# Kernel tuning notes

Measured on AMD Instinct MI355X. Metric: run time of the kernel, lower is better.

Reference implementation:

```python
import jax, jax.numpy as jnp
import numpy as np


def setup_inputs() -> dict:
    key = jax.random.key(0)
    ks = jax.random.split(key, 5)
    B, S, D = 2, 2048, 1024
    inv = 1.0 / np.sqrt(D)
    inp = {
        "x": jax.random.normal(ks[0], (B, S, D), jnp.float32),
        "Wq": jax.random.normal(ks[1], (D, D), jnp.float32) * inv,
        "bq": jnp.zeros((D,), jnp.float32),
        "Wk": jax.random.normal(ks[2], (D, D), jnp.float32) * inv,
        "bk": jnp.zeros((D,), jnp.float32),
        "Wv": jax.random.normal(ks[3], (D, D), jnp.float32) * inv,
        "bv": jnp.zeros((D,), jnp.float32),
        "Wo": jax.random.normal(ks[4], (D, D), jnp.float32) * inv,
        "bo": jnp.zeros((D,), jnp.float32),
        "num_heads": 16,
        "window_size": 128,
    }
    return inp


def reference(x, Wq, bq, Wk, bk, Wv, bv, Wo, bo, num_heads, window_size):
    B, S, D = x.shape
    H = num_heads
    hd = D // H
    scale = 1.0 / np.sqrt(hd)

    def split_heads(t):  # [B,S,D] -> [B,H,S,hd]
        return t.reshape(B, S, H, hd).transpose(0, 2, 1, 3)

    q = split_heads(x @ Wq + bq)
    k = split_heads(x @ Wk + bk)
    v = split_heads(x @ Wv + bv)

    # dense scores, then sliding-window + causal mask (faithful to original)
    scores = jnp.einsum('bhqd,bhkd->bhqk', q, k) * scale  # [B,H,S,S]
    i = jnp.arange(S)[:, None]
    j = jnp.arange(S)[None, :]
    # position i attends to j in [i - window_size + 1, i]
    mask = (j <= i) & (j > i - window_size)
    scores = jnp.where(mask, scores, -jnp.inf)
    attn_weights = jax.nn.softmax(scores, axis=-1)  # dropout is identity in eval

    out = jnp.einsum('bhqk,bhkd->bhqd', attn_weights, v)  # [B,H,S,hd]
    out = out.transpose(0, 2, 1, 3).reshape(B, S, D)
    return out @ Wo + bo, attn_weights
```

## Files before the change

### kernel.cpp

```cpp
#include <hip/hip_runtime.h>
#include <cmath>

typedef __attribute__((ext_vector_type(8))) __bf16 v8bf;
typedef __attribute__((ext_vector_type(4))) float  v4f;

#define DEV static __device__ __forceinline__

DEV unsigned short f2bf(float f) {
  unsigned u = __builtin_bit_cast(unsigned, f);
  unsigned r = u + 0x7fffu + ((u >> 16) & 1u);
  return (unsigned short)(r >> 16);
}
DEV float bf2f(unsigned short s) {
  return __builtin_bit_cast(float, ((unsigned)s) << 16);
}
DEV v8bf ld8(const unsigned short* p) { return *(const v8bf*)p; }

DEV void gl16(const unsigned short* g, unsigned short* l) {
  __builtin_amdgcn_global_load_lds(
      (const __attribute__((address_space(1))) unsigned int*)g,
      (__attribute__((address_space(3))) unsigned int*)l, 16, 0, 0);
}

__global__ __launch_bounds__(256) void k_prep(const float* __restrict__ x,
                                              const float* __restrict__ Wq,
                                              const float* __restrict__ Wk,
                                              const float* __restrict__ Wv,
                                              const float* __restrict__ Wo,
                                              const float* __restrict__ bq,
                                              const float* __restrict__ bk,
                                              const float* __restrict__ bv,
                                              unsigned short* __restrict__ xb,
                                              unsigned short* __restrict__ WT,
                                              unsigned short* __restrict__ WoT,
                                              float* __restrict__ bqkv) {
  __shared__ float t[32][33];
  int bx = blockIdx.x, tid = threadIdx.x;
  if (bx < 4096) {
    int i = bx * 256 + tid;
    float4 v = ((const float4*)x)[i];
    unsigned lo = (unsigned)f2bf(v.x) | ((unsigned)f2bf(v.y) << 16);
    unsigned hi = (unsigned)f2bf(v.z) | ((unsigned)f2bf(v.w) << 16);
    ((uint2*)xb)[i] = make_uint2(lo, hi);
  } else if (bx < 8192) {
    int rem = bx - 4096;
    int z = rem >> 10, r2 = rem & 1023;
    const float* src = (z == 0) ? Wq : (z == 1) ? Wk : (z == 2) ? Wv : Wo;
    unsigned short* dst = (z < 3) ? WT + z * 1048576 : WoT;
    int n0 = (r2 & 31) * 32, k0 = (r2 >> 5) * 32;
    int tx = tid & 31, ty = tid >> 5;
    for (int r = ty; r < 32; r += 8)
      t[r][tx] = src[(k0 + r) * 1024 + n0 + tx];
    __syncthreads();
    for (int r = ty; r < 32; r += 8)
      dst[(n0 + r) * 1024 + k0 + tx] = f2bf(t[tx][r]);
  } else {
    int i = (bx - 8192) * 256 + tid;
    float v = (i < 1024) ? bq[i] : (i < 2048 ? bk[i - 1024] : bv[i - 2048]);
    bqkv[i] = v;
  }
}

__global__ __launch_bounds__(256) void k_gemm1(const unsigned short* __restrict__ A,
                                               const unsigned short* __restrict__ Bt,
                                               const float* __restrict__ bias,
                                               unsigned short* __restrict__ Cout) {
  constexpr int K = 1024;
  __shared__ __attribute__((aligned(16))) unsigned short As[128 * 32];
  __shared__ __attribute__((aligned(16))) unsigned short Bs[128 * 32];
  int tid = threadIdx.x;
  int wave = tid >> 6, lane = tid & 63;
  int m0 = blockIdx.y * 128, n0 = blockIdx.x * 128;
  int wm = (wave >> 1) * 64, wn = (wave & 1) * 64;
  int m = lane & 15, q4 = lane >> 4;
  int arow = tid >> 2, acol = (tid & 3) * 8;
  v4f acc[4][4] = {};
  const unsigned short* ga0 = A + (m0 + arow) * K + acol;
  const unsigned short* ga1 = A + (m0 + 64 + arow) * K + acol;
  const unsigned short* gb0 = Bt + (n0 + arow) * K + acol;
  const unsigned short* gb1 = Bt + (n0 + 64 + arow) * K + acol;
  unsigned short* lA0 = As + wave * 512;
  unsigned short* lA1 = As + 2048 + wave * 512;
  unsigned short* lB0 = Bs + wave * 512;
  unsigned short* lB1 = Bs + 2048 + wave * 512;

  for (int kt = 0; kt < K; kt += 32) {
    gl16(ga0 + kt, lA0);
    gl16(ga1 + kt, lA1);
    gl16(gb0 + kt, lB0);
    gl16(gb1 + kt, lB1);
    __syncthreads();
    v8bf af[4], bfv[4];
#pragma unroll
    for (int mt = 0; mt < 4; mt++) af[mt] = ld8(&As[(wm + mt * 16 + m) * 32 + q4 * 8]);
#pragma unroll
    for (int nt = 0; nt < 4; nt++) bfv[nt] = ld8(&Bs[(wn + nt * 16 + m) * 32 + q4 * 8]);
#pragma unroll
    for (int mt = 0; mt < 4; mt++)
#pragma unroll
      for (int nt = 0; nt < 4; nt++)
        acc[mt][nt] = __builtin_amdgcn_mfma_f32_16x16x32_bf16(af[mt], bfv[nt], acc[mt][nt], 0, 0, 0);
    __syncthreads();
  }
#pragma unroll
  for (int mt = 0; mt < 4; mt++)
#pragma unroll
    for (int nt = 0; nt < 4; nt++) {
      int col = n0 + wn + nt * 16 + m;
      float bb = bias[col];
#pragma unroll
      for (int r = 0; r < 4; r++) {
        int row = m0 + wm + mt * 16 + q4 * 4 + r;
        Cout[row * 3072 + col] = f2bf(acc[mt][nt][r] + bb);
      }
    }
}

__global__ __launch_bounds__(256) void k_transv(const unsigned short* __restrict__ QKV,
                                                unsigned short* __restrict__ Vtg) {
  __shared__ unsigned short t[32][33];
  int bx = blockIdx.x, tid = threadIdx.x;
  int st = bx & 63, h2 = (bx >> 6) & 1, bh = bx >> 7;
  int b = bh >> 4, h = bh & 15;
  int s0 = st * 32, d0 = h2 * 32;
  int tx = tid & 31, ty = tid >> 5;
  const unsigned short* src = QKV + (size_t)b * 2048 * 3072 + 2048 + h * 64 + d0;
  for (int r = ty; r < 32; r += 8)
    t[r][tx] = src[(size_t)(s0 + r) * 3072 + tx];
  __syncthreads();
  unsigned short* dst = Vtg + (size_t)(bh * 64 + d0) * 2048 + s0;
  for (int r = ty; r < 32; r += 8)
    dst[(size_t)r * 2048 + tx] = t[tx][r];
}

__global__ __launch_bounds__(256) void k_attn(const unsigned short* __restrict__ QKV,
                                              const unsigned short* __restrict__ Vtg,
                                              unsigned short* __restrict__ Oatt,
                                              unsigned short* __restrict__ cb) {
  constexpr int VTS = 208;
  constexpr int PSS = 168;
  __shared__ __attribute__((aligned(16))) unsigned short Vt[64 * VTS];
  __shared__ __attribute__((aligned(16))) unsigned short Ps[4][16 * PSS];
  int b = blockIdx.z, h = blockIdx.y, i0 = blockIdx.x * 64;
  int tid = threadIdx.x, wave = tid >> 6, lane = tid & 63;
  int kbase = i0 - 128;
  const int ld = 3072;
  const unsigned short* Qg = QKV + b * 2048 * ld + h * 64;
  const unsigned short* Kg = Qg + 1024;

  const unsigned short* vsrc = Vtg + (size_t)(b * 16 + h) * 64 * 2048;
  for (int idx = tid; idx < 1536; idx += 256) {
    int row = idx / 24, c16 = idx % 24;
    int gcol = kbase + c16 * 8;
    if (gcol < 0) gcol = 0;
    v8bf vv = ld8(vsrc + (size_t)row * 2048 + gcol);
    *(v8bf*)&Vt[row * VTS + c16 * 8] = vv;
  }
  {
    int row = tid >> 2, c4 = (tid & 3) * 4;
    *(uint2*)&Vt[row * VTS + 192 + c4] = make_uint2(0u, 0u);
  }
  for (int c = lane; c < 16 * 24; c += 64)
    Ps[wave][(c / 24) * PSS + 144 + (c % 24)] = 0;
  __syncthreads();

  int qb = i0 + wave * 16;
  int m = lane & 15, q4 = lane >> 4;

  const unsigned short* qrow = Qg + (qb + m) * ld;
  v8bf qa0 = ld8(qrow + q4 * 8);
  v8bf qa1 = ld8(qrow + 32 + q4 * 8);

  v4f sc[9];
#pragma unroll
  for (int n = 0; n < 9; n++) {
    int key = kbase + wave * 16 + n * 16 + m;
    int kg = key < 0 ? 0 : key;
    const unsigned short* krow = Kg + kg * ld;
    v8bf kb0 = ld8(krow + q4 * 8);
    v8bf kb1 = ld8(krow + 32 + q4 * 8);
    v4f z = {0.f, 0.f, 0.f, 0.f};
    z = __builtin_amdgcn_mfma_f32_16x16x32_bf16(qa0, kb0, z, 0, 0, 0);
    z = __builtin_amdgcn_mfma_f32_16x16x32_bf16(qa1, kb1, z, 0, 0, 0);
    sc[n] = z;
  }
  float mx[4] = {-3e38f, -3e38f, -3e38f, -3e38f};
#pragma unroll
  for (int n = 0; n < 9; n++)
#pragma unroll
    for (int r = 0; r < 4; r++) {
      int i = qb + q4 * 4 + r;
      int j = kbase + wave * 16 + n * 16 + m;
      float v = sc[n][r] * 0.125f;
      bool ok = (j >= 0) && (j <= i) && (j > i - 128);
      v = ok ? v : -3e38f;
      sc[n][r] = v;
      mx[r] = fmaxf(mx[r], v);
    }
#pragma unroll
  for (int o = 1; o < 16; o <<= 1)
#pragma unroll
    for (int r = 0; r < 4; r++) mx[r] = fmaxf(mx[r], __shfl_xor(mx[r], o, 64));
  float sum[4] = {0.f, 0.f, 0.f, 0.f};
#pragma unroll
  for (int n = 0; n < 9; n++)
#pragma unroll
    for (int r = 0; r < 4; r++) {
      float p = __expf(sc[n][r] - mx[r]);
      sc[n][r] = p;
      sum[r] += p;
    }
#pragma unroll
  for (int o = 1; o < 16; o <<= 1)
#pragma unroll
    for (int r = 0; r < 4; r++) sum[r] += __shfl_xor(sum[r], o, 64);
  float inv[4];
#pragma unroll
  for (int r = 0; r < 4; r++) inv[r] = 1.0f / sum[r];

#pragma unroll
  for (int n = 0; n < 9; n++)
#pragma unroll
    for (int r = 0; r < 4; r++)
      Ps[wave][(q4 * 4 + r) * PSS + n * 16 + m] = f2bf(sc[n][r] * inv[r]);
  __syncthreads();

  v4f oacc[4] = {};
#pragma unroll
  for (int c = 0; c < 5; c++) {
    v8bf pa = ld8(&Ps[wave][m * PSS + c * 32 + q4 * 8]);
#pragma unroll
    for (int dt = 0; dt < 4; dt++) {
      v8bf vb = ld8(&Vt[(dt * 16 + m) * VTS + wave * 16 + c * 32 + q4 * 8]);
      oacc[dt] = __builtin_amdgcn_mfma_f32_16x16x32_bf16(pa, vb, oacc[dt], 0, 0, 0);
    }
  }
#pragma unroll
  for (int dt = 0; dt < 4; dt++)
#pragma unroll
    for (int r = 0; r < 4; r++)
      Oatt[(b * 2048 + qb + q4 * 4 + r) * 1024 + h * 64 + dt * 16 + m] = f2bf(oacc[dt][r]);

  for (int R = 0; R < 16; R++) {
    int row = (b * 16 + h) * 2048 + qb + R;
    unsigned short p0 = Ps[wave][R * PSS + R + 1 + lane * 2];
    unsigned short p1 = Ps[wave][R * PSS + R + 2 + lane * 2];
    ((unsigned*)cb)[row * 64 + lane] = (unsigned)p0 | ((unsigned)p1 << 16);
  }
}

__global__ __launch_bounds__(256) void k_tail(const unsigned short* __restrict__ Oat,
                                              const unsigned short* __restrict__ WoT,
                                              const float* __restrict__ bo,
                                              float* __restrict__ out,
                                              const unsigned short* __restrict__ cb,
                                              float* __restrict__ wout) {
  __shared__ __attribute__((aligned(16))) unsigned short As[128 * 32];
  __shared__ __attribute__((aligned(16))) unsigned short Bs[128 * 32];
  int tid = threadIdx.x, wave = tid >> 6, lane = tid & 63;

  if (blockIdx.x < 256) {
    constexpr int K = 1024;
    int bx = blockIdx.x;
    int n0 = (bx & 7) * 128, m0 = (bx >> 3) * 128;
    int wm = (wave >> 1) * 64, wn = (wave & 1) * 64;
    int m = lane & 15, q4 = lane >> 4;
    int arow = tid >> 2, acol = (tid & 3) * 8;
    v4f acc[4][4] = {};
    const unsigned short* ga0 = Oat + (m0 + arow) * K + acol;
    const unsigned short* ga1 = Oat + (m0 + 64 + arow) * K + acol;
    const unsigned short* gb0 = WoT + (n0 + arow) * K + acol;
    const unsigned short* gb1 = WoT + (n0 + 64 + arow) * K + acol;
    unsigned short* lA0 = As + wave * 512;
    unsigned short* lA1 = As + 2048 + wave * 512;
    unsigned short* lB0 = Bs + wave * 512;
    unsigned short* lB1 = Bs + 2048 + wave * 512;
    for (int kt = 0; kt < K; kt += 32) {
      gl16(ga0 + kt, lA0);
      gl16(ga1 + kt, lA1);
      gl16(gb0 + kt, lB0);
      gl16(gb1 + kt, lB1);
      __syncthreads();
      v8bf af[4], bfv[4];
#pragma unroll
      for (int mt = 0; mt < 4; mt++) af[mt] = ld8(&As[(wm + mt * 16 + m) * 32 + q4 * 8]);
#pragma unroll
      for (int nt = 0; nt < 4; nt++) bfv[nt] = ld8(&Bs[(wn + nt * 16 + m) * 32 + q4 * 8]);
#pragma unroll
      for (int mt = 0; mt < 4; mt++)
#pragma unroll
        for (int nt = 0; nt < 4; nt++)
          acc[mt][nt] = __builtin_amdgcn_mfma_f32_16x16x32_bf16(af[mt], bfv[nt], acc[mt][nt], 0, 0, 0);
      __syncthreads();
    }
#pragma unroll
    for (int mt = 0; mt < 4; mt++)
#pragma unroll
      for (int nt = 0; nt < 4; nt++) {
        int col = n0 + wn + nt * 16 + m;
        float bb = bo[col];
#pragma unroll
        for (int r = 0; r < 4; r++) {
          int row = m0 + wm + mt * 16 + q4 * 4 + r;
          out[row * 1024 + col] = acc[mt][nt][r] + bb;
        }
      }
  } else {
    int wb = blockIdx.x - 256;
    int rbase = wb * 16 + wave * 4;
    for (int rr = 0; rr < 4; rr++) {
      int row = rbase + rr;
      int i = row & 2047;
      float* rowp = wout + (size_t)row * 2048;
      const unsigned short* crow = cb + (size_t)row * 128;
      int lo = i - 127;
#pragma unroll
      for (int it = 0; it < 8; it++) {
        int col = it * 256 + lane * 4;
        v4f v = {0.f, 0.f, 0.f, 0.f};
        if (col <= i && col + 3 >= lo) {
#pragma unroll
          for (int e = 0; e < 4; e++) {
            int j = col + e;
            if (j >= lo && j <= i && j >= 0)
              v[e] = bf2f(crow[j - lo]);
          }
        }
        __builtin_nontemporal_store(v, (v4f*)(rowp + col));
      }
    }
  }
}

extern "C" void kernel_launch(void* const* d_in, const int* in_sizes, int n_in,
                              void* d_out, int out_size, void* d_ws, size_t ws_size,
                              hipStream_t stream) {
  (void)in_sizes; (void)n_in; (void)out_size; (void)ws_size;
  const float* x  = (const float*)d_in[0];
  const float* Wq = (const float*)d_in[1];
  const float* bq = (const float*)d_in[2];
  const float* Wk = (const float*)d_in[3];
  const float* bk = (const float*)d_in[4];
  const float* Wv = (const float*)d_in[5];
  const float* bv = (const float*)d_in[6];
  const float* Wo = (const float*)d_in[7];
  const float* bo = (const float*)d_in[8];

  char* ws = (char*)d_ws;
  unsigned short* xb   = (unsigned short*)(ws);
  unsigned short* WT   = (unsigned short*)(ws + 8388608);
  unsigned short* WoT  = (unsigned short*)(ws + 14680064);
  float*          bqkv = (float*)(ws + 16777216);
  unsigned short* QKV  = (unsigned short*)(ws + 16789504);
  unsigned short* Oat  = (unsigned short*)(ws + 41955328);
  unsigned short* cb   = (unsigned short*)(ws + 50343936);
  unsigned short* Vtg  = (unsigned short*)(ws + 67121152);

  float* out  = (float*)d_out;
  float* wout = out + 4194304;

  k_prep<<<8204, 256, 0, stream>>>(x, Wq, Wk, Wv, Wo, bq, bk, bv, xb, WT, WoT, bqkv);
  k_gemm1<<<dim3(24, 32), 256, 0, stream>>>(xb, WT, bqkv, QKV);
  k_transv<<<4096, 256, 0, stream>>>(QKV, Vtg);
  k_attn<<<dim3(32, 16, 2), 256, 0, stream>>>(QKV, Vtg, Oat, cb);
  k_tail<<<4352, 256, 0, stream>>>(Oat, WoT, bo, out, cb, wout);
}
```

Before: 640.9 us.

## Spread attention-weight zero fill across GEMM and attention kernels, write band directly

Zeroing of the dense 2x16x2048x2048 attention-weight output is split into row chunks. Those chunks are interleaved as extra blocks in the QKV GEMM, the attention kernel and the output projection, so the zero stores overlap with compute instead of running as a separate phase. The attention kernel now writes its band probabilities straight into the final fp32 output, which removes the compressed intermediate buffer and its re-read. The trade-offs are more complex block-index mapping, scattered scalar stores for the band, and partial-vector element stores at band edges.

Result: no change. 653.4 us (+1.9%).

```diff
diff --git a/kernel.cpp b/kernel.cpp
--- a/kernel.cpp
+++ b/kernel.cpp
@@ -20,6 +20,33 @@
   __builtin_amdgcn_global_load_lds(
       (const __attribute__((address_space(1))) unsigned int*)g,
       (__attribute__((address_space(3))) unsigned int*)l, 16, 0, 0);
+}
+
+DEV void zero_rows(float* __restrict__ wout, int rbase, int wave, int lane) {
+  int r0 = rbase + wave * 4;
+  for (int rr = 0; rr < 4; rr++) {
+    int row = r0 + rr;
+    int i = row & 2047;
+    int lo = i - 127;
+    float* rowp = wout + (size_t)row * 2048;
+#pragma unroll
+    for (int it = 0; it < 8; it++) {
+      int col = it * 256 + lane * 4;
+      bool full_in = (col >= lo) && (col + 3 <= i);
+      if (full_in) continue;
+      bool overlap = (col + 3 >= lo) && (col <= i);
+      if (!overlap) {
+        v4f z = {0.f, 0.f, 0.f, 0.f};
+        __builtin_nontemporal_store(z, (v4f*)(rowp + col));
+      } else {
+#pragma unroll
+        for (int e = 0; e < 4; e++) {
+          int j = col + e;
+          if (j < lo || j > i) rowp[j] = 0.f;
+        }
+      }
+    }
+  }
 }
 
 __global__ __launch_bounds__(256) void k_prep(const float* __restrict__ x,
@@ -64,13 +91,21 @@
 __global__ __launch_bounds__(256) void k_gemm1(const unsigned short* __restrict__ A,
                                                const unsigned short* __restrict__ Bt,
                                                const float* __restrict__ bias,
-                                               unsigned short* __restrict__ Cout) {
+                                               unsigned short* __restrict__ Cout,
+                                               float* __restrict__ wout) {
   constexpr int K = 1024;
   __shared__ __attribute__((aligned(16))) unsigned short As[128 * 32];
   __shared__ __attribute__((aligned(16))) unsigned short Bs[128 * 32];
   int tid = threadIdx.x;
   int wave = tid >> 6, lane = tid & 63;
-  int m0 = blockIdx.y * 128, n0 = blockIdx.x * 128;
+  int bx = blockIdx.x;
+  if (!(bx % 3 == 0 && bx < 2304)) {
+    int wid = (bx < 2304) ? (bx - (bx + 2) / 3) : (1536 + bx - 2304);
+    zero_rows(wout, wid * 16, wave, lane);
+    return;
+  }
+  int gid = bx / 3;
+  int n0 = (gid % 24) * 128, m0 = (gid / 24) * 128;
   int wm = (wave >> 1) * 64, wn = (wave & 1) * 64;
   int m = lane & 15, q4 = lane >> 4;
   int arow = tid >> 2, acol = (tid & 3) * 8;
@@ -136,13 +171,19 @@
 __global__ __launch_bounds__(256) void k_attn(const unsigned short* __restrict__ QKV,
                                               const unsigned short* __restrict__ Vtg,
                                               unsigned short* __restrict__ Oatt,
-                                              unsigned short* __restrict__ cb) {
+                                              float* __restrict__ wout) {
   constexpr int VTS = 208;
   constexpr int PSS = 168;
   __shared__ __attribute__((aligned(16))) unsigned short Vt[64 * VTS];
   __shared__ __attribute__((aligned(16))) unsigned short Ps[4][16 * PSS];
-  int b = blockIdx.z, h = blockIdx.y, i0 = blockIdx.x * 64;
   int tid = threadIdx.x, wave = tid >> 6, lane = tid & 63;
+  int bx = blockIdx.x;
+  if (bx >= 32) {
+    int wid = (bx - 32) + 40 * (blockIdx.y + 16 * blockIdx.z);
+    zero_rows(wout, 28672 + wid * 16, wave, lane);
+    return;
+  }
+  int b = blockIdx.z, h = blockIdx.y, i0 = bx * 64;
   int kbase = i0 - 128;
   const int ld = 3072;
   const unsigned short* Qg = QKV + b * 2048 * ld + h * 64;
@@ -242,10 +283,15 @@
       Oatt[(b * 2048 + qb + q4 * 4 + r) * 1024 + h * 64 + dt * 16 + m] = f2bf(oacc[dt][r]);
 
   for (int R = 0; R < 16; R++) {
-    int row = (b * 16 + h) * 2048 + qb + R;
-    unsigned short p0 = Ps[wave][R * PSS + R + 1 + lane * 2];
-    unsigned short p1 = Ps[wave][R * PSS + R + 2 + lane * 2];
-    ((unsigned*)cb)[row * 64 + lane] = (unsigned)p0 | ((unsigned)p1 << 16);
+    int iq = qb + R;
+    float* rowp = wout + (size_t)((b * 16 + h) * 2048 + iq) * 2048;
+    int lo = iq - 127;
+    int t0 = R + 1 + lane * 2;
+    float p0 = bf2f(Ps[wave][R * PSS + t0]);
+    float p1 = bf2f(Ps[wave][R * PSS + t0 + 1]);
+    int j0 = lo + lane * 2;
+    if (j0 >= 0) rowp[j0] = p0;
+    if (j0 + 1 >= 0) rowp[j0 + 1] = p1;
   }
 }
 
@@ -253,83 +299,62 @@
                                               const unsigned short* __restrict__ WoT,
                                               const float* __restrict__ bo,
                                               float* __restrict__ out,
-                                              const unsigned short* __restrict__ cb,
                                               float* __restrict__ wout) {
   __shared__ __attribute__((aligned(16))) unsigned short As[128 * 32];
   __shared__ __attribute__((aligned(16))) unsigned short Bs[128 * 32];
   int tid = threadIdx.x, wave = tid >> 6, lane = tid & 63;
-
-  if (blockIdx.x < 256) {
-    constexpr int K = 1024;
-    int bx = blockIdx.x;
-    int n0 = (bx & 7) * 128, m0 = (bx >> 3) * 128;
-    int wm = (wave >> 1) * 64, wn = (wave & 1) * 64;
-    int m = lane & 15, q4 = lane >> 4;
-    int arow = tid >> 2, acol = (tid & 3) * 8;
-    v4f acc[4][4] = {};
-    const unsigned short* ga0 = Oat + (m0 + arow) * K + acol;
-    const unsigned short* ga1 = Oat + (m0 + 64 + arow) * K + acol;
-    const unsigned short* gb0 = WoT + (n0 + arow) * K + acol;
-    const unsigned short* gb1 = WoT + (n0 + 64 + arow) * K + acol;
-    unsigned short* lA0 = As + wave * 512;
-    unsigned short* lA1 = As + 2048 + wave * 512;
-    unsigned short* lB0 = Bs + wave * 512;
-    unsigned short* lB1 = Bs + 2048 + wave * 512;
-    for (int kt = 0; kt < K; kt += 32) {
-      gl16(ga0 + kt, lA0);
-      gl16(ga1 + kt, lA1);
-      gl16(gb0 + kt, lB0);
-      gl16(gb1 + kt, lB1);
-      __syncthreads();
-      v8bf af[4], bfv[4];
-#pragma unroll
-      for (int mt = 0; mt < 4; mt++) af[mt] = ld8(&As[(wm + mt * 16 + m) * 32 + q4 * 8]);
-#pragma unroll
-      for (int nt = 0; nt < 4; nt++) bfv[nt] = ld8(&Bs[(wn + nt * 16 + m) * 32 + q4 * 8]);
-#pragma unroll
-      for (int mt = 0; mt < 4; mt++)
-#pragma unroll
-        for (int nt = 0; nt < 4; nt++)
-          acc[mt][nt] = __builtin_amdgcn_mfma_f32_16x16x32_bf16(af[mt], bfv[nt], acc[mt][nt], 0, 0, 0);
-      __syncthreads();
-    }
+  int bx = blockIdx.x;
+
+  if (bx % 5 != 0) {
+    int wid = bx - (bx + 4) / 5;
+    zero_rows(wout, 49152 + wid * 16, wave, lane);
+    return;
+  }
+  constexpr int K = 1024;
+  int gid = bx / 5;
+  int n0 = (gid & 7) * 128, m0 = (gid >> 3) * 128;
+  int wm = (wave >> 1) * 64, wn = (wave & 1) * 64;
+  int m = lane & 15, q4 = lane >> 4;
+  int arow = tid >> 2, acol = (tid & 3) * 8;
+  v4f acc[4][4] = {};
+  const unsigned short* ga0 = Oat + (m0 + arow) * K + acol;
+  const unsigned short* ga1 = Oat + (m0 + 64 + arow) * K + acol;
+  const unsigned short* gb0 = WoT + (n0 + arow) * K + acol;
+  const unsigned short* gb1 = WoT + (n0 + 64 + arow) * K + acol;
+  unsigned short* lA0 = As + wave * 512;
+  unsigned short* lA1 = As + 2048 + wave * 512;
+  unsigned short* lB0 = Bs + wave * 512;
+  unsigned short* lB1 = Bs + 2048 + wave * 512;
+  for (int kt = 0; kt < K; kt += 32) {
+    gl16(ga0 + kt, lA0);
+    gl16(ga1 + kt, lA1);
+    gl16(gb0 + kt, lB0);
+    gl16(gb1 + kt, lB1);
+    __syncthreads();
+    v8bf af[4], bfv[4];
+#pragma unroll
+    for (int mt = 0; mt < 4; mt++) af[mt] = ld8(&As[(wm + mt * 16 + m) * 32 + q4 * 8]);
+#pragma unroll
+    for (int nt = 0; nt < 4; nt++) bfv[nt] = ld8(&Bs[(wn + nt * 16 + m) * 32 + q4 * 8]);
 #pragma unroll
     for (int mt = 0; mt < 4; mt++)
 #pragma unroll
-      for (int nt = 0; nt < 4; nt++) {
-        int col = n0 + wn + nt * 16 + m;
-        float bb = bo[col];
-#pragma unroll
-        for (int r = 0; r < 4; r++) {
-          int row = m0 + wm + mt * 16 + q4 * 4 + r;
-          out[row * 1024 + col] = acc[mt][nt][r] + bb;
-        }
+      for (int nt = 0; nt < 4; nt++)
+        acc[mt][nt] = __builtin_amdgcn_mfma_f32_16x16x32_bf16(af[mt], bfv[nt], acc[mt][nt], 0, 0, 0);
+    __syncthreads();
+  }
+#pragma unroll
+  for (int mt = 0; mt < 4; mt++)
+#pragma unroll
+    for (int nt = 0; nt < 4; nt++) {
+      int col = n0 + wn + nt * 16 + m;
+      float bb = bo[col];
+#pragma unroll
+      for (int r = 0; r < 4; r++) {
+        int row = m0 + wm + mt * 16 + q4 * 4 + r;
+        out[row * 1024 + col] = acc[mt][nt][r] + bb;
       }
-  } else {
-    int wb = blockIdx.x - 256;
-    int rbase = wb * 16 + wave * 4;
-    for (int rr = 0; rr < 4; rr++) {
-      int row = rbase + rr;
-      int i = row & 2047;
-      float* rowp = wout + (size_t)row * 2048;
-      const unsigned short* crow = cb + (size_t)row * 128;
-      int lo = i - 127;
-#pragma unroll
-      for (int it = 0; it < 8; it++) {
-        int col = it * 256 + lane * 4;
-        v4f v = {0.f, 0.f, 0.f, 0.f};
-        if (col <= i && col + 3 >= lo) {
-#pragma unroll
-          for (int e = 0; e < 4; e++) {
-            int j = col + e;
-            if (j >= lo && j <= i && j >= 0)
-              v[e] = bf2f(crow[j - lo]);
-          }
-        }
-        __builtin_nontemporal_store(v, (v4f*)(rowp + col));
-      }
-    }
-  }
+    }
 }
 
 extern "C" void kernel_launch(void* const* d_in, const int* in_sizes, int n_in,
@@ -353,15 +378,14 @@
   float*          bqkv = (float*)(ws + 16777216);
   unsigned short* QKV  = (unsigned short*)(ws + 16789504);
   unsigned short* Oat  = (unsigned short*)(ws + 41955328);
-  unsigned short* cb   = (unsigned short*)(ws + 50343936);
   unsigned short* Vtg  = (unsigned short*)(ws + 67121152);
 
   float* out  = (float*)d_out;
   float* wout = out + 4194304;
 
   k_prep<<<8204, 256, 0, stream>>>(x, Wq, Wk, Wv, Wo, bq, bk, bv, xb, WT, WoT, bqkv);
-  k_gemm1<<<dim3(24, 32), 256, 0, stream>>>(xb, WT, bqkv, QKV);
+  k_gemm1<<<2560, 256, 0, stream>>>(xb, WT, bqkv, QKV, wout);
   k_transv<<<4096, 256, 0, stream>>>(QKV, Vtg);
-  k_attn<<<dim3(32, 16, 2), 256, 0, stream>>>(QKV, Vtg, Oat, cb);
-  k_tail<<<4352, 256, 0, stream>>>(Oat, WoT, bo, out, cb, wout);
-}
+  k_attn<<<dim3(72, 16, 2), 256, 0, stream>>>(QKV, Vtg, Oat, wout);
+  k_tail<<<1280, 256, 0, stream>>>(Oat, WoT, bo, out, wout);
+}
```
